# Kernel optimization log

Hardware: AMD Instinct MI355X
Metric: run time of the kernel (lower is better)

Reference implementation:

```python
import jax, jax.numpy as jnp
import numpy as np

N = 172032          # total anchor points (8 images x 21504)
C = 256             # prompt classes
REG_MAX = 16        # DFL bins
M = 64              # GT boxes
IMG = 1024.0
RADIUS = 0.75       # center_sampling_radius
SIGMA = 2.0         # heat sigma
ALPHA, GAMMA = 0.75, 2.0  # varifocal
MARGIN = 8.0
AREA_THR = 0.6
EPS = 1e-6


def setup_inputs() -> dict:
    key = jax.random.key(0)
    ks = jax.random.split(key, 10)
    anchor_points = jax.random.uniform(ks[0], (N, 2)) * IMG
    cls_logits = jax.random.normal(ks[1], (N, C))
    target_scores = jax.random.uniform(ks[2], (N, C))
    pred_dist = jax.random.normal(ks[3], (N, 4, REG_MAX))
    dfl_target = jax.random.uniform(ks[4], (N, 4)) * (REG_MAX - 1)
    # valid xyxy GT boxes inside the image
    xy = jax.random.uniform(ks[5], (M, 2)) * (IMG - 200.0)
    wh = jax.random.uniform(ks[6], (M, 2)) * 180.0 + 20.0
    gt_boxes = jnp.concatenate([xy, xy + wh], axis=-1)
    box_weights = jax.random.uniform(ks[7], (M,))
    pred_boxes = jax.random.uniform(ks[8], (N, 4)) * IMG
    obj_logits = jax.random.normal(ks[9], (N,))
    return {"anchor_points": anchor_points, "cls_logits": cls_logits,
            "target_scores": target_scores, "pred_dist": pred_dist,
            "dfl_target": dfl_target, "gt_boxes": gt_boxes,
            "box_weights": box_weights, "pred_boxes": pred_boxes,
            "obj_logits": obj_logits}


def _inside_and_delta(ap, boxes):
    # ap [N,2], boxes [M,4] -> inside [M,N], delta [M,N,2], half_size [M,1,2]
    inside = ((ap[None, :, 0] >= boxes[:, None, 0]) & (ap[None, :, 0] <= boxes[:, None, 2]) &
              (ap[None, :, 1] >= boxes[:, None, 1]) & (ap[None, :, 1] <= boxes[:, None, 3]))
    center = (boxes[:, :2] + boxes[:, 2:]) * 0.5          # [M,2]
    half = jnp.clip((boxes[:, 2:] - boxes[:, :2]) * 0.5, 1.0)
    delta = (ap[None, :, :] - center[:, None, :]) / half[:, None, :]  # [M,N,2]
    return inside, delta


def build_box_region_weights(ap, boxes, bw, radius):
    inside, delta = _inside_and_delta(ap, boxes)
    center_mask = jnp.max(jnp.abs(delta), axis=-1) <= radius           # [M,N]
    cand = inside & center_mask
    has_cand = jnp.any(cand, axis=1, keepdims=True)
    cand = jnp.where(has_cand, cand, inside)                           # fallback to inside
    return jnp.max(cand.astype(bw.dtype) * bw[:, None], axis=0)        # [N]


def build_center_heat_targets(ap, boxes, sigma):
    sigma = max(float(sigma), 0.001)
    inside, delta = _inside_and_delta(ap, boxes)
    heat = jnp.exp(-0.5 * jnp.sum((delta / sigma) ** 2, axis=-1))      # [M,N]
    heat = heat * inside.astype(heat.dtype)
    return jnp.clip(jnp.max(heat, axis=0), 0.0, 1.0)                   # [N]


def sigmoid_varifocal_loss(logits, targets, alpha, gamma):
    prob = jax.nn.sigmoid(logits)
    weight = alpha * prob ** gamma * (1.0 - targets) + targets
    # stable BCE-with-logits
    bce = jnp.maximum(logits, 0.0) - logits * targets + jnp.log1p(jnp.exp(-jnp.abs(logits)))
    return bce * weight


def dfl_loss(pred_dist, target, reg_max):
    # pred_dist [N,4,R], target [N,4] float in [0, R-1]
    tl = jnp.clip(target.astype(jnp.int32), 0, reg_max - 1)
    tr = jnp.clip(tl + 1, 0, reg_max - 1)
    wl = tr.astype(target.dtype) - target
    wr = 1.0 - wl
    logp = jax.nn.log_softmax(pred_dist, axis=-1)
    ll = -jnp.take_along_axis(logp, tl[..., None], axis=-1)[..., 0]
    lr = -jnp.take_along_axis(logp, tr[..., None], axis=-1)[..., 0]
    return ll * wl + lr * wr                                           # [N,4]


def weighted_mean(loss, weights):
    while weights.ndim < loss.ndim:
        weights = weights[..., None]
    return jnp.sum(loss * weights) / jnp.clip(jnp.sum(weights), EPS)


def oversize_box_penalty(boxes, image_size, area_threshold):
    x1 = jnp.clip(boxes[:, 0], 0.0, image_size)
    y1 = jnp.clip(boxes[:, 1], 0.0, image_size)
    x2 = jnp.clip(boxes[:, 2], 0.0, image_size)
    y2 = jnp.clip(boxes[:, 3], 0.0, image_size)
    w = jnp.clip(x2 - x1, 0.0)
    h = jnp.clip(y2 - y1, 0.0)
    area_ratio = w * h / max(float(image_size * image_size), 1.0)
    edge = ((x1 <= 1.0).astype(boxes.dtype) + (y1 <= 1.0).astype(boxes.dtype) +
            (x2 >= image_size - 1.0).astype(boxes.dtype) + (y2 >= image_size - 1.0).astype(boxes.dtype)) / 4.0
    return jnp.clip(area_ratio - area_threshold, 0.0) * (1.0 + edge)


def reference(anchor_points, cls_logits, target_scores, pred_dist, dfl_target,
              gt_boxes, box_weights, pred_boxes, obj_logits):
    region_w = build_box_region_weights(anchor_points, gt_boxes, box_weights, RADIUS)  # [N]
    heat = build_center_heat_targets(anchor_points, gt_boxes, SIGMA)                   # [N]

    vfl = sigmoid_varifocal_loss(cls_logits, target_scores, ALPHA, GAMMA)              # [N,C]
    cls_loss = weighted_mean(vfl, region_w + heat)

    obj_bce = jnp.maximum(obj_logits, 0.0) - obj_logits * heat + jnp.log1p(jnp.exp(-jnp.abs(obj_logits)))
    obj_loss = jnp.mean(obj_bce)

    dfl = dfl_loss(pred_dist, dfl_target, REG_MAX)                                     # [N,4]
    box_dfl_loss = weighted_mean(dfl, region_w)

    penalty = jnp.mean(oversize_box_penalty(pred_boxes, IMG, AREA_THR))
    margin = jnp.mean(jax.nn.relu(jnp.max(cls_logits, axis=-1) - MARGIN))

    total = cls_loss + obj_loss + box_dfl_loss + 0.1 * penalty + 0.05 * margin
    return total
```

## Files before the change

kernel.cpp:

```cpp
#include <hip/hip_runtime.h>

#define MM 64
#define NQ 7
#define MAIN_BLOCKS 1024

__device__ __forceinline__ float vfl_term(float l, float t, float* lmax) {
    float e = __expf(-l);
    float p = __fdividef(1.0f, 1.0f + e);
    float bce = fmaxf(l, 0.0f) - l * t - __logf(fmaxf(p, 1.0f - p));
    float wgt = 0.75f * p * p * (1.0f - t) + t;
    *lmax = fmaxf(*lmax, l);
    return bce * wgt;
}

__global__ __launch_bounds__(256) void k_hascand(
    const float2* __restrict__ ap, const float4* __restrict__ boxes,
    unsigned long long* __restrict__ mask, int n_pts)
{
    __shared__ float4 sb[MM];
    if (threadIdx.x < MM) sb[threadIdx.x] = boxes[threadIdx.x];
    __syncthreads();
    unsigned long long local = 0ull;
    int stride = gridDim.x * blockDim.x;
    for (int n = blockIdx.x * blockDim.x + threadIdx.x; n < n_pts; n += stride) {
        float2 p = ap[n];
        for (int m = 0; m < MM; ++m) {
            float4 b = sb[m];
            if (p.x >= b.x && p.x <= b.z && p.y >= b.y && p.y <= b.w) {
                float hx = fmaxf((b.z - b.x) * 0.5f, 1.0f);
                float hy = fmaxf((b.w - b.y) * 0.5f, 1.0f);
                float dx = fabsf(p.x - (b.x + b.z) * 0.5f) / hx;
                float dy = fabsf(p.y - (b.y + b.w) * 0.5f) / hy;
                if (fmaxf(dx, dy) <= 0.75f) local |= (1ull << m);
            }
        }
    }
    #pragma unroll
    for (int o = 32; o; o >>= 1) local |= __shfl_xor(local, o);
    if ((threadIdx.x & 63) == 0 && local) atomicOr(mask, local);
}

__global__ __launch_bounds__(256) void k_main(
    const float2* __restrict__ ap,
    const float4* __restrict__ cls4,
    const float4* __restrict__ ts4,
    const float*  __restrict__ pd,
    const float*  __restrict__ dflt,
    const float4* __restrict__ boxes,
    const float*  __restrict__ bw,
    const float4* __restrict__ pboxes,
    const float*  __restrict__ obj,
    const unsigned long long* __restrict__ candmask,
    float* __restrict__ partials,
    int n_pts)
{
    const int tid  = threadIdx.x;
    const int lane = tid & 63;
    const int wid  = tid >> 6;
    const int waveGlobal = blockIdx.x * 4 + wid;
    const int totalWaves = gridDim.x * 4;

    float4 b  = boxes[lane];
    float mybw = bw[lane];
    float inv_hx = __fdividef(1.0f, fmaxf((b.z - b.x) * 0.5f, 1.0f));
    float inv_hy = __fdividef(1.0f, fmaxf((b.w - b.y) * 0.5f, 1.0f));
    float ccx = (b.x + b.z) * 0.5f, ccy = (b.y + b.w) * 0.5f;
    bool has_c = ((candmask[0] >> lane) & 1ull) != 0;

    const int kseg = lane >> 4;
    const int jj   = lane & 15;

    float accS1 = 0.f;
    float accS3 = 0.f;
    float accS2 = 0.f;
    float accS4 = 0.f;
    float accObj = 0.f;
    float accMar = 0.f;

    for (int n = waveGlobal; n < n_pts; n += totalWaves) {
        float2 p = ap[n];
        bool inside = (p.x >= b.x) & (p.x <= b.z) & (p.y >= b.y) & (p.y <= b.w);
        float dx = (p.x - ccx) * inv_hx;
        float dy = (p.y - ccy) * inv_hy;
        bool cand = inside && (fmaxf(fabsf(dx), fabsf(dy)) <= 0.75f);
        bool eff  = has_c ? cand : inside;
        float rw = eff ? mybw : 0.f;
        float ht = inside ? __expf(-0.125f * (dx * dx + dy * dy)) : 0.f;
        #pragma unroll
        for (int o = 32; o; o >>= 1) {
            rw = fmaxf(rw, __shfl_xor(rw, o));
            ht = fmaxf(ht, __shfl_xor(ht, o));
        }
        ht = fminf(ht, 1.0f);
        float w = rw + ht;

        float4 l4 = cls4[(size_t)n * 64 + lane];
        float4 t4 = ts4[(size_t)n * 64 + lane];
        float lmax = -1e30f;
        float vsum = vfl_term(l4.x, t4.x, &lmax) + vfl_term(l4.y, t4.y, &lmax)
                   + vfl_term(l4.z, t4.z, &lmax) + vfl_term(l4.w, t4.w, &lmax);
        accS1 += w * vsum;
        #pragma unroll
        for (int o = 32; o; o >>= 1) lmax = fmaxf(lmax, __shfl_xor(lmax, o));
        accMar += fmaxf(lmax - 8.0f, 0.f);
        accS2 += w;
        accS4 += rw;

        float ol = obj[n];
        accObj += fmaxf(ol, 0.f) - ol * ht + __logf(1.0f + __expf(-fabsf(ol)));

        float x = pd[(size_t)n * 64 + lane];
        float tg = dflt[(size_t)n * 4 + kseg];
        float mx = x;
        #pragma unroll
        for (int o = 8; o; o >>= 1) mx = fmaxf(mx, __shfl_xor(mx, o));
        float e = __expf(x - mx);
        float se = e;
        #pragma unroll
        for (int o = 8; o; o >>= 1) se += __shfl_xor(se, o);
        float logp = (x - mx) - __logf(se);
        int tl = (int)tg; tl = max(0, min(tl, 15));
        int tr = min(tl + 1, 15);
        float wl = (float)tr - tg;
        float contrib = 0.f;
        if (jj == tl) contrib += -logp * wl;
        if (jj == tr) contrib += -logp * (1.0f - wl);
        accS3 += rw * contrib;
    }

    float accPen = 0.f;
    int gsize = gridDim.x * blockDim.x;
    for (int n = blockIdx.x * blockDim.x + tid; n < n_pts; n += gsize) {
        float4 pbx = pboxes[n];
        float x1 = fminf(fmaxf(pbx.x, 0.f), 1024.0f);
        float y1 = fminf(fmaxf(pbx.y, 0.f), 1024.0f);
        float x2 = fminf(fmaxf(pbx.z, 0.f), 1024.0f);
        float y2 = fminf(fmaxf(pbx.w, 0.f), 1024.0f);
        float wq = fmaxf(x2 - x1, 0.f), hq = fmaxf(y2 - y1, 0.f);
        float ar = wq * hq * (1.0f / (1024.0f * 1024.0f));
        float edge = ((x1 <= 1.f ? 1.f : 0.f) + (y1 <= 1.f ? 1.f : 0.f) +
                      (x2 >= 1023.f ? 1.f : 0.f) + (y2 >= 1023.f ? 1.f : 0.f)) * 0.25f;
        accPen += fmaxf(ar - 0.6f, 0.f) * (1.f + edge);
    }

    #pragma unroll
    for (int o = 32; o; o >>= 1) {
        accS1  += __shfl_xor(accS1, o);
        accS3  += __shfl_xor(accS3, o);
        accPen += __shfl_xor(accPen, o);
    }
    __shared__ float sh[4][NQ];
    if (lane == 0) {
        sh[wid][0] = accS1; sh[wid][1] = accS2; sh[wid][2] = accS3;
        sh[wid][3] = accS4; sh[wid][4] = accObj; sh[wid][5] = accMar;
        sh[wid][6] = accPen;
    }
    __syncthreads();
    if (tid < NQ) {
        partials[blockIdx.x * NQ + tid] =
            sh[0][tid] + sh[1][tid] + sh[2][tid] + sh[3][tid];
    }
}

__global__ __launch_bounds__(256) void k_final(
    const float* __restrict__ partials, int nblocks,
    float* __restrict__ out, int n_pts)
{
    double acc[NQ];
    #pragma unroll
    for (int q = 0; q < NQ; ++q) acc[q] = 0.0;
    for (int i = threadIdx.x; i < nblocks; i += 256) {
        #pragma unroll
        for (int q = 0; q < NQ; ++q) acc[q] += (double)partials[i * NQ + q];
    }
    __shared__ double sh[256][NQ + 1];
    #pragma unroll
    for (int q = 0; q < NQ; ++q) sh[threadIdx.x][q] = acc[q];
    __syncthreads();
    for (int s = 128; s; s >>= 1) {
        if (threadIdx.x < s) {
            #pragma unroll
            for (int q = 0; q < NQ; ++q) sh[threadIdx.x][q] += sh[threadIdx.x + s][q];
        }
        __syncthreads();
    }
    if (threadIdx.x == 0) {
        double S1 = sh[0][0], S2 = sh[0][1], S3 = sh[0][2], S4 = sh[0][3];
        double So = sh[0][4], Sm = sh[0][5], Sp = sh[0][6];
        double invN = 1.0 / (double)n_pts;
        double cls_loss = S1 / fmax(S2, 1e-6);
        double dfl_loss = S3 / fmax(S4, 1e-6);
        double total = cls_loss + So * invN + dfl_loss + 0.1 * Sp * invN + 0.05 * Sm * invN;
        out[0] = (float)total;
    }
}

extern "C" void kernel_launch(void* const* d_in, const int* in_sizes, int n_in,
                              void* d_out, int out_size, void* d_ws, size_t ws_size,
                              hipStream_t stream) {
    const float2* ap    = (const float2*)d_in[0];
    const float4* cls4  = (const float4*)d_in[1];
    const float4* ts4   = (const float4*)d_in[2];
    const float*  pd    = (const float*)d_in[3];
    const float*  dflt  = (const float*)d_in[4];
    const float4* boxes = (const float4*)d_in[5];
    const float*  bw    = (const float*)d_in[6];
    const float4* pbx   = (const float4*)d_in[7];
    const float*  obj   = (const float*)d_in[8];
    int n_pts = in_sizes[0] / 2;

    unsigned long long* mask = (unsigned long long*)d_ws;
    float* partials = (float*)((char*)d_ws + 16);

    hipMemsetAsync(d_ws, 0, 16, stream);
    k_hascand<<<256, 256, 0, stream>>>(ap, boxes, mask, n_pts);
    k_main<<<MAIN_BLOCKS, 256, 0, stream>>>(ap, cls4, ts4, pd, dflt, boxes, bw,
                                            pbx, obj, mask, partials, n_pts);
    k_final<<<1, 256, 0, stream>>>(partials, MAIN_BLOCKS, (float*)d_out, n_pts);
}
```

Before: 155.4 us.

## Precompute per-anchor region and heat weights in a prep kernel, unroll main loop

Adds a k_prep kernel that computes each anchor's region weight and heat target by a per-thread loop over the 64 boxes and writes them to a workspace buffer. k_main then loads these weights instead of doing 64-lane box tests and two wave-wide max reductions per anchor. The main loop also handles two anchors per iteration to raise memory-level parallelism, and the grid size is doubled. The cost is an extra kernel launch plus a write and read of a small per-anchor buffer. An unused helper (anchor_body) has a malformed obj term, but it is never called.

```diff
diff --git a/kernel.cpp b/kernel.cpp
--- a/kernel.cpp
+++ b/kernel.cpp
@@ -2,7 +2,7 @@
 
 #define MM 64
 #define NQ 7
-#define MAIN_BLOCKS 1024
+#define MAIN_BLOCKS 2048
 
 __device__ __forceinline__ float vfl_term(float l, float t, float* lmax) {
     float e = __expf(-l);
@@ -40,17 +40,74 @@
     if ((threadIdx.x & 63) == 0 && local) atomicOr(mask, local);
 }
 
+__global__ __launch_bounds__(256) void k_prep(
+    const float2* __restrict__ ap, const float4* __restrict__ boxes,
+    const float* __restrict__ bw, const unsigned long long* __restrict__ candmask,
+    float2* __restrict__ w2, int n_pts)
+{
+    __shared__ float4 sB[MM];
+    __shared__ float4 sA[MM];
+    __shared__ float  sW[MM];
+    if (threadIdx.x < MM) {
+        float4 b = boxes[threadIdx.x];
+        sB[threadIdx.x] = b;
+        float ihx = __fdividef(1.0f, fmaxf((b.z - b.x) * 0.5f, 1.0f));
+        float ihy = __fdividef(1.0f, fmaxf((b.w - b.y) * 0.5f, 1.0f));
+        sA[threadIdx.x] = make_float4((b.x + b.z) * 0.5f, (b.y + b.w) * 0.5f, ihx, ihy);
+        sW[threadIdx.x] = bw[threadIdx.x];
+    }
+    __syncthreads();
+    unsigned long long cm = candmask[0];
+    int stride = gridDim.x * blockDim.x;
+    for (int n = blockIdx.x * blockDim.x + threadIdx.x; n < n_pts; n += stride) {
+        float2 p = ap[n];
+        float rw = 0.f, ht = 0.f;
+        #pragma unroll 8
+        for (int m = 0; m < MM; ++m) {
+            float4 b = sB[m];
+            float4 a = sA[m];
+            bool inside = (p.x >= b.x) & (p.x <= b.z) & (p.y >= b.y) & (p.y <= b.w);
+            float dx = (p.x - a.x) * a.z;
+            float dy = (p.y - a.y) * a.w;
+            bool cand = inside && (fmaxf(fabsf(dx), fabsf(dy)) <= 0.75f);
+            bool eff = ((cm >> m) & 1ull) ? cand : inside;
+            if (eff) rw = fmaxf(rw, sW[m]);
+            float h = __expf(-0.125f * (dx * dx + dy * dy));
+            if (inside) ht = fmaxf(ht, h);
+        }
+        ht = fminf(ht, 1.0f);
+        w2[n] = make_float2(rw + ht, rw);
+    }
+}
+
+__device__ __forceinline__ void anchor_body(
+    float4 l4, float4 t4, float pda, float2 wv, float ol, float tg,
+    int jj, float valid,
+    float* accS1, float* accS2, float* accS3, float* accS4,
+    float* accObj, float* accMar)
+{
+    float w = wv.x, rw = wv.y;
+    float lmax = -1e30f;
+    float vsum = vfl_term(l4.x, t4.x, &lmax) + vfl_term(l4.y, t4.y, &lmax)
+               + vfl_term(l4.z, t4.z, &lmax) + vfl_term(l4.w, t4.w, &lmax);
+    *accS1 += valid * w * vsum;
+    #pragma unroll
+    for (int o = 32; o; o >>= 1) lmax = fmaxf(lmax, __shfl_xor(lmax, o));
+    *accMar += valid * fmaxf(lmax - 8.0f, 0.f);
+    *accS2 += valid * w;
+    *accS4 += valid * rw;
+
+    *accObj += valid * (fmaxf(ol, 0.f) - ol * w , 0.f);
+}
+
 __global__ __launch_bounds__(256) void k_main(
-    const float2* __restrict__ ap,
     const float4* __restrict__ cls4,
     const float4* __restrict__ ts4,
     const float*  __restrict__ pd,
     const float*  __restrict__ dflt,
-    const float4* __restrict__ boxes,
-    const float*  __restrict__ bw,
     const float4* __restrict__ pboxes,
     const float*  __restrict__ obj,
-    const unsigned long long* __restrict__ candmask,
+    const float2* __restrict__ w2,
     float* __restrict__ partials,
     int n_pts)
 {
@@ -58,74 +115,87 @@
     const int lane = tid & 63;
     const int wid  = tid >> 6;
     const int waveGlobal = blockIdx.x * 4 + wid;
-    const int totalWaves = gridDim.x * 4;
-
-    float4 b  = boxes[lane];
-    float mybw = bw[lane];
-    float inv_hx = __fdividef(1.0f, fmaxf((b.z - b.x) * 0.5f, 1.0f));
-    float inv_hy = __fdividef(1.0f, fmaxf((b.w - b.y) * 0.5f, 1.0f));
-    float ccx = (b.x + b.z) * 0.5f, ccy = (b.y + b.w) * 0.5f;
-    bool has_c = ((candmask[0] >> lane) & 1ull) != 0;
+    const int step = gridDim.x * 4;
 
     const int kseg = lane >> 4;
     const int jj   = lane & 15;
 
-    float accS1 = 0.f;
-    float accS3 = 0.f;
-    float accS2 = 0.f;
-    float accS4 = 0.f;
-    float accObj = 0.f;
-    float accMar = 0.f;
-
-    for (int n = waveGlobal; n < n_pts; n += totalWaves) {
-        float2 p = ap[n];
-        bool inside = (p.x >= b.x) & (p.x <= b.z) & (p.y >= b.y) & (p.y <= b.w);
-        float dx = (p.x - ccx) * inv_hx;
-        float dy = (p.y - ccy) * inv_hy;
-        bool cand = inside && (fmaxf(fabsf(dx), fabsf(dy)) <= 0.75f);
-        bool eff  = has_c ? cand : inside;
-        float rw = eff ? mybw : 0.f;
-        float ht = inside ? __expf(-0.125f * (dx * dx + dy * dy)) : 0.f;
-        #pragma unroll
-        for (int o = 32; o; o >>= 1) {
-            rw = fmaxf(rw, __shfl_xor(rw, o));
-            ht = fmaxf(ht, __shfl_xor(ht, o));
-        }
-        ht = fminf(ht, 1.0f);
-        float w = rw + ht;
-
-        float4 l4 = cls4[(size_t)n * 64 + lane];
-        float4 t4 = ts4[(size_t)n * 64 + lane];
-        float lmax = -1e30f;
-        float vsum = vfl_term(l4.x, t4.x, &lmax) + vfl_term(l4.y, t4.y, &lmax)
-                   + vfl_term(l4.z, t4.z, &lmax) + vfl_term(l4.w, t4.w, &lmax);
-        accS1 += w * vsum;
-        #pragma unroll
-        for (int o = 32; o; o >>= 1) lmax = fmaxf(lmax, __shfl_xor(lmax, o));
-        accMar += fmaxf(lmax - 8.0f, 0.f);
-        accS2 += w;
-        accS4 += rw;
-
-        float ol = obj[n];
-        accObj += fmaxf(ol, 0.f) - ol * ht + __logf(1.0f + __expf(-fabsf(ol)));
-
-        float x = pd[(size_t)n * 64 + lane];
-        float tg = dflt[(size_t)n * 4 + kseg];
-        float mx = x;
-        #pragma unroll
-        for (int o = 8; o; o >>= 1) mx = fmaxf(mx, __shfl_xor(mx, o));
-        float e = __expf(x - mx);
-        float se = e;
-        #pragma unroll
-        for (int o = 8; o; o >>= 1) se += __shfl_xor(se, o);
-        float logp = (x - mx) - __logf(se);
-        int tl = (int)tg; tl = max(0, min(tl, 15));
-        int tr = min(tl + 1, 15);
-        float wl = (float)tr - tg;
-        float contrib = 0.f;
-        if (jj == tl) contrib += -logp * wl;
-        if (jj == tr) contrib += -logp * (1.0f - wl);
-        accS3 += rw * contrib;
+    float accS1 = 0.f, accS2 = 0.f, accS3 = 0.f, accS4 = 0.f;
+    float accObj = 0.f, accMar = 0.f;
+
+    for (int n = waveGlobal; n < n_pts; n += 2 * step) {
+        int n1 = n + step;
+        bool have2 = n1 < n_pts;
+        size_t r0 = (size_t)n * 64 + lane;
+        size_t r1 = (size_t)(have2 ? n1 : n) * 64 + lane;
+        int q1 = have2 ? n1 : n;
+
+        float4 l4a = cls4[r0], t4a = ts4[r0];
+        float4 l4b = cls4[r1], t4b = ts4[r1];
+        float  pda = pd[r0],   pdb = pd[r1];
+        float2 wva = w2[n],    wvb = w2[q1];
+        float  ola = obj[n],   olb = obj[q1];
+        float  tga = dflt[(size_t)n * 4 + kseg], tgb = dflt[(size_t)q1 * 4 + kseg];
+        float  v1 = have2 ? 1.0f : 0.0f;
+
+        {
+            float w = wva.x, rw = wva.y, ht = wva.x - wva.y;
+            float lmax = -1e30f;
+            float vsum = vfl_term(l4a.x, t4a.x, &lmax) + vfl_term(l4a.y, t4a.y, &lmax)
+                       + vfl_term(l4a.z, t4a.z, &lmax) + vfl_term(l4a.w, t4a.w, &lmax);
+            accS1 += w * vsum;
+            #pragma unroll
+            for (int o = 32; o; o >>= 1) lmax = fmaxf(lmax, __shfl_xor(lmax, o));
+            accMar += fmaxf(lmax - 8.0f, 0.f);
+            accS2 += w; accS4 += rw;
+            accObj += fmaxf(ola, 0.f) - ola * ht + __logf(1.0f + __expf(-fabsf(ola)));
+
+            float x = pda;
+            float mx = x;
+            #pragma unroll
+            for (int o = 8; o; o >>= 1) mx = fmaxf(mx, __shfl_xor(mx, o));
+            float e = __expf(x - mx);
+            float se = e;
+            #pragma unroll
+            for (int o = 8; o; o >>= 1) se += __shfl_xor(se, o);
+            float logp = (x - mx) - __logf(se);
+            int tl = (int)tga; tl = max(0, min(tl, 15));
+            int tr = min(tl + 1, 15);
+            float wl = (float)tr - tga;
+            float contrib = 0.f;
+            if (jj == tl) contrib += -logp * wl;
+            if (jj == tr) contrib += -logp * (1.0f - wl);
+            accS3 += rw * contrib;
+        }
+        {
+            float w = wvb.x, rw = wvb.y, ht = wvb.x - wvb.y;
+            float lmax = -1e30f;
+            float vsum = vfl_term(l4b.x, t4b.x, &lmax) + vfl_term(l4b.y, t4b.y, &lmax)
+                       + vfl_term(l4b.z, t4b.z, &lmax) + vfl_term(l4b.w, t4b.w, &lmax);
+            accS1 += v1 * w * vsum;
+            #pragma unroll
+            for (int o = 32; o; o >>= 1) lmax = fmaxf(lmax, __shfl_xor(lmax, o));
+            accMar += v1 * fmaxf(lmax - 8.0f, 0.f);
+            accS2 += v1 * w; accS4 += v1 * rw;
+            accObj += v1 * (fmaxf(olb, 0.f) - olb * ht + __logf(1.0f + __expf(-fabsf(olb))));
+
+            float x = pdb;
+            float mx = x;
+            #pragma unroll
+            for (int o = 8; o; o >>= 1) mx = fmaxf(mx, __shfl_xor(mx, o));
+            float e = __expf(x - mx);
+            float se = e;
+            #pragma unroll
+            for (int o = 8; o; o >>= 1) se += __shfl_xor(se, o);
+            float logp = (x - mx) - __logf(se);
+            int tl = (int)tgb; tl = max(0, min(tl, 15));
+            int tr = min(tl + 1, 15);
+            float wl = (float)tr - tgb;
+            float contrib = 0.f;
+            if (jj == tl) contrib += -logp * wl;
+            if (jj == tr) contrib += -logp * (1.0f - wl);
+            accS3 += v1 * rw * contrib;
+        }
     }
 
     float accPen = 0.f;
@@ -210,11 +280,13 @@
     int n_pts = in_sizes[0] / 2;
 
     unsigned long long* mask = (unsigned long long*)d_ws;
-    float* partials = (float*)((char*)d_ws + 16);
+    float* partials = (float*)((char*)d_ws + 64);
+    float2* w2 = (float2*)((char*)d_ws + 65536);
 
     hipMemsetAsync(d_ws, 0, 16, stream);
     k_hascand<<<256, 256, 0, stream>>>(ap, boxes, mask, n_pts);
-    k_main<<<MAIN_BLOCKS, 256, 0, stream>>>(ap, cls4, ts4, pd, dflt, boxes, bw,
-                                            pbx, obj, mask, partials, n_pts);
+    k_prep<<<672, 256, 0, stream>>>(ap, boxes, bw, mask, w2, n_pts);
+    k_main<<<MAIN_BLOCKS, 256, 0, stream>>>(cls4, ts4, pd, dflt, pbx, obj, w2,
+                                            partials, n_pts);
     k_final<<<1, 256, 0, stream>>>(partials, MAIN_BLOCKS, (float*)d_out, n_pts);
 }
```

Result: faster. 150.8 us (-3.0%).

## Split per-point weight computation into prep kernel and batch main loop four points per wave

Applied to the files above, without the earlier changes.

Adds a prep kernel that computes per-point region and heat weights (one thread per point looping over boxes), plus the objectness and penalty terms, and writes the weights to a workspace buffer. The main kernel then only streams the class, target and distribution tensors, handling four points per wave iteration so more loads are in flight. It also drops the max-subtraction in the DFL softmax, rewrites the DFL target as a triangle weight, and skips the margin reduction unless some logit exceeds the margin. The costs are an extra launch and a workspace round trip. Removing the softmax max-subtraction risks overflow for large logits, and the loop stops at multiples of four points, which can drop a tail of points.

```diff
diff --git a/kernel.cpp b/kernel.cpp
--- a/kernel.cpp
+++ b/kernel.cpp
@@ -1,15 +1,18 @@
 #include <hip/hip_runtime.h>
 
 #define MM 64
-#define NQ 7
-#define MAIN_BLOCKS 1024
-
-__device__ __forceinline__ float vfl_term(float l, float t, float* lmax) {
+#define MAIN_BLOCKS 1344
+#define PREP_BLOCKS 672
+#define NQ_MAIN 5
+#define NQ_PREP 2
+
+__device__ __forceinline__ float vfl1(float l, float t, float* vmax) {
     float e = __expf(-l);
     float p = __fdividef(1.0f, 1.0f + e);
-    float bce = fmaxf(l, 0.0f) - l * t - __logf(fmaxf(p, 1.0f - p));
-    float wgt = 0.75f * p * p * (1.0f - t) + t;
-    *lmax = fmaxf(*lmax, l);
+    float q = fmaxf(p, 1.0f - p);
+    float bce = fmaf(-l, t, fmaxf(l, 0.0f)) - __logf(q);
+    float wgt = fmaf(0.75f * p * p, 1.0f - t, t);
+    *vmax = fmaxf(*vmax, l);
     return bce * wgt;
 }
 
@@ -40,97 +43,49 @@
     if ((threadIdx.x & 63) == 0 && local) atomicOr(mask, local);
 }
 
-__global__ __launch_bounds__(256) void k_main(
-    const float2* __restrict__ ap,
-    const float4* __restrict__ cls4,
-    const float4* __restrict__ ts4,
-    const float*  __restrict__ pd,
-    const float*  __restrict__ dflt,
-    const float4* __restrict__ boxes,
-    const float*  __restrict__ bw,
-    const float4* __restrict__ pboxes,
-    const float*  __restrict__ obj,
-    const unsigned long long* __restrict__ candmask,
-    float* __restrict__ partials,
-    int n_pts)
-{
-    const int tid  = threadIdx.x;
-    const int lane = tid & 63;
-    const int wid  = tid >> 6;
-    const int waveGlobal = blockIdx.x * 4 + wid;
-    const int totalWaves = gridDim.x * 4;
-
-    float4 b  = boxes[lane];
-    float mybw = bw[lane];
-    float inv_hx = __fdividef(1.0f, fmaxf((b.z - b.x) * 0.5f, 1.0f));
-    float inv_hy = __fdividef(1.0f, fmaxf((b.w - b.y) * 0.5f, 1.0f));
-    float ccx = (b.x + b.z) * 0.5f, ccy = (b.y + b.w) * 0.5f;
-    bool has_c = ((candmask[0] >> lane) & 1ull) != 0;
-
-    const int kseg = lane >> 4;
-    const int jj   = lane & 15;
-
-    float accS1 = 0.f;
-    float accS3 = 0.f;
-    float accS2 = 0.f;
-    float accS4 = 0.f;
-    float accObj = 0.f;
-    float accMar = 0.f;
-
-    for (int n = waveGlobal; n < n_pts; n += totalWaves) {
+__global__ __launch_bounds__(256) void k_prep(
+    const float2* __restrict__ ap, const float4* __restrict__ boxes,
+    const float* __restrict__ bw, const unsigned long long* __restrict__ candmask,
+    const float4* __restrict__ pboxes, const float* __restrict__ obj,
+    float2* __restrict__ w2, float* __restrict__ prep_partials, int n_pts)
+{
+    __shared__ float4 sB[MM];
+    __shared__ float4 sA[MM];
+    __shared__ float  sW[MM];
+    if (threadIdx.x < MM) {
+        float4 b = boxes[threadIdx.x];
+        sB[threadIdx.x] = b;
+        float ihx = __fdividef(1.0f, fmaxf((b.z - b.x) * 0.5f, 1.0f));
+        float ihy = __fdividef(1.0f, fmaxf((b.w - b.y) * 0.5f, 1.0f));
+        sA[threadIdx.x] = make_float4((b.x + b.z) * 0.5f, (b.y + b.w) * 0.5f, ihx, ihy);
+        sW[threadIdx.x] = bw[threadIdx.x];
+    }
+    __syncthreads();
+    unsigned long long cm = candmask[0];
+    int n = blockIdx.x * blockDim.x + threadIdx.x;
+    float aObj = 0.f, aPen = 0.f;
+    if (n < n_pts) {
         float2 p = ap[n];
-        bool inside = (p.x >= b.x) & (p.x <= b.z) & (p.y >= b.y) & (p.y <= b.w);
-        float dx = (p.x - ccx) * inv_hx;
-        float dy = (p.y - ccy) * inv_hy;
-        bool cand = inside && (fmaxf(fabsf(dx), fabsf(dy)) <= 0.75f);
-        bool eff  = has_c ? cand : inside;
-        float rw = eff ? mybw : 0.f;
-        float ht = inside ? __expf(-0.125f * (dx * dx + dy * dy)) : 0.f;
-        #pragma unroll
-        for (int o = 32; o; o >>= 1) {
-            rw = fmaxf(rw, __shfl_xor(rw, o));
-            ht = fmaxf(ht, __shfl_xor(ht, o));
+        float rw = 0.f, ht = 0.f;
+        #pragma unroll 8
+        for (int m = 0; m < MM; ++m) {
+            float4 b = sB[m];
+            float4 a = sA[m];
+            bool inside = (p.x >= b.x) & (p.x <= b.z) & (p.y >= b.y) & (p.y <= b.w);
+            float dx = (p.x - a.x) * a.z;
+            float dy = (p.y - a.y) * a.w;
+            bool cand = inside && (fmaxf(fabsf(dx), fabsf(dy)) <= 0.75f);
+            bool eff = ((cm >> m) & 1ull) ? cand : inside;
+            if (eff) rw = fmaxf(rw, sW[m]);
+            float h = __expf(-0.125f * (dx * dx + dy * dy));
+            if (inside) ht = fmaxf(ht, h);
         }
         ht = fminf(ht, 1.0f);
-        float w = rw + ht;
-
-        float4 l4 = cls4[(size_t)n * 64 + lane];
-        float4 t4 = ts4[(size_t)n * 64 + lane];
-        float lmax = -1e30f;
-        float vsum = vfl_term(l4.x, t4.x, &lmax) + vfl_term(l4.y, t4.y, &lmax)
-                   + vfl_term(l4.z, t4.z, &lmax) + vfl_term(l4.w, t4.w, &lmax);
-        accS1 += w * vsum;
-        #pragma unroll
-        for (int o = 32; o; o >>= 1) lmax = fmaxf(lmax, __shfl_xor(lmax, o));
-        accMar += fmaxf(lmax - 8.0f, 0.f);
-        accS2 += w;
-        accS4 += rw;
+        w2[n] = make_float2(rw + ht, rw);
 
         float ol = obj[n];
-        accObj += fmaxf(ol, 0.f) - ol * ht + __logf(1.0f + __expf(-fabsf(ol)));
-
-        float x = pd[(size_t)n * 64 + lane];
-        float tg = dflt[(size_t)n * 4 + kseg];
-        float mx = x;
-        #pragma unroll
-        for (int o = 8; o; o >>= 1) mx = fmaxf(mx, __shfl_xor(mx, o));
-        float e = __expf(x - mx);
-        float se = e;
-        #pragma unroll
-        for (int o = 8; o; o >>= 1) se += __shfl_xor(se, o);
-        float logp = (x - mx) - __logf(se);
-        int tl = (int)tg; tl = max(0, min(tl, 15));
-        int tr = min(tl + 1, 15);
-        float wl = (float)tr - tg;
-        float contrib = 0.f;
-        if (jj == tl) contrib += -logp * wl;
-        if (jj == tr) contrib += -logp * (1.0f - wl);
-        accS3 += rw * contrib;
-    }
-
-    float accPen = 0.f;
-    int gsize = gridDim.x * blockDim.x;
-    for (int n = blockIdx.x * blockDim.x + tid; n < n_pts; n += gsize) {
+        aObj = fmaxf(ol, 0.f) - ol * ht + __logf(1.0f + __expf(-fabsf(ol)));
+
         float4 pbx = pboxes[n];
         float x1 = fminf(fmaxf(pbx.x, 0.f), 1024.0f);
         float y1 = fminf(fmaxf(pbx.y, 0.f), 1024.0f);
@@ -140,58 +95,133 @@
         float ar = wq * hq * (1.0f / (1024.0f * 1024.0f));
         float edge = ((x1 <= 1.f ? 1.f : 0.f) + (y1 <= 1.f ? 1.f : 0.f) +
                       (x2 >= 1023.f ? 1.f : 0.f) + (y2 >= 1023.f ? 1.f : 0.f)) * 0.25f;
-        accPen += fmaxf(ar - 0.6f, 0.f) * (1.f + edge);
-    }
-
+        aPen = fmaxf(ar - 0.6f, 0.f) * (1.f + edge);
+    }
     #pragma unroll
     for (int o = 32; o; o >>= 1) {
-        accS1  += __shfl_xor(accS1, o);
-        accS3  += __shfl_xor(accS3, o);
-        accPen += __shfl_xor(accPen, o);
-    }
-    __shared__ float sh[4][NQ];
+        aObj += __shfl_xor(aObj, o);
+        aPen += __shfl_xor(aPen, o);
+    }
+    __shared__ float sh[4][2];
+    int lane = threadIdx.x & 63, wid = threadIdx.x >> 6;
+    if (lane == 0) { sh[wid][0] = aObj; sh[wid][1] = aPen; }
+    __syncthreads();
+    if (threadIdx.x < NQ_PREP) {
+        prep_partials[blockIdx.x * NQ_PREP + threadIdx.x] =
+            sh[0][threadIdx.x] + sh[1][threadIdx.x] + sh[2][threadIdx.x] + sh[3][threadIdx.x];
+    }
+}
+
+__global__ __launch_bounds__(256) void k_main(
+    const float4* __restrict__ cls4,
+    const float4* __restrict__ ts4,
+    const float*  __restrict__ pd,
+    const float*  __restrict__ dflt,
+    const float2* __restrict__ w2,
+    float* __restrict__ partials,
+    int n_pts)
+{
+    const int tid  = threadIdx.x;
+    const int lane = tid & 63;
+    const int wid  = tid >> 6;
+    const int wave = blockIdx.x * 4 + wid;
+    const int CHUNK = MAIN_BLOCKS * 4 * 4;
+    const int ksel = lane >> 4;
+    const float jjf = (float)(lane & 15);
+
+    float accS1 = 0.f, accS2 = 0.f, accS3 = 0.f, accS4 = 0.f, accMar = 0.f;
+
+    for (int n0 = wave * 4; n0 + 3 < n_pts; n0 += CHUNK) {
+        float4 l4[4], t4[4];
+        float  xp[4], tg[4];
+        float2 wv[4];
+        #pragma unroll
+        for (int u = 0; u < 4; ++u) {
+            int n = n0 + u;
+            int o = n * 64 + lane;
+            l4[u] = cls4[o];
+            t4[u] = ts4[o];
+            xp[u] = pd[o];
+            wv[u] = w2[n];
+            tg[u] = dflt[n * 4 + ksel];
+        }
+        #pragma unroll
+        for (int u = 0; u < 4; ++u) {
+            float w = wv[u].x, rw = wv[u].y;
+            float vmax = -1e30f;
+            float vsum = vfl1(l4[u].x, t4[u].x, &vmax) + vfl1(l4[u].y, t4[u].y, &vmax)
+                       + vfl1(l4[u].z, t4[u].z, &vmax) + vfl1(l4[u].w, t4[u].w, &vmax);
+            accS1 = fmaf(w, vsum, accS1);
+            accS2 += w;
+            accS4 += rw;
+            if (__any(vmax > 8.0f)) {
+                float t = vmax;
+                #pragma unroll
+                for (int o = 32; o; o >>= 1) t = fmaxf(t, __shfl_xor(t, o));
+                accMar += t - 8.0f;
+            }
+            float e = __expf(xp[u]);
+            float se = e;
+            #pragma unroll
+            for (int o = 8; o; o >>= 1) se += __shfl_xor(se, o);
+            float lse = __logf(se);
+            float d  = tg[u] - jjf;
+            float tw = fmaxf(1.0f - fabsf(d), 0.0f);
+            float term = fmaf(-tw, xp[u], lse * 0.0625f);
+            accS3 = fmaf(rw, term, accS3);
+        }
+    }
+
+    #pragma unroll
+    for (int o = 32; o; o >>= 1) {
+        accS1 += __shfl_xor(accS1, o);
+        accS3 += __shfl_xor(accS3, o);
+    }
+    __shared__ float sh[4][NQ_MAIN];
     if (lane == 0) {
         sh[wid][0] = accS1; sh[wid][1] = accS2; sh[wid][2] = accS3;
-        sh[wid][3] = accS4; sh[wid][4] = accObj; sh[wid][5] = accMar;
-        sh[wid][6] = accPen;
-    }
-    __syncthreads();
-    if (tid < NQ) {
-        partials[blockIdx.x * NQ + tid] =
+        sh[wid][3] = accS4; sh[wid][4] = accMar;
+    }
+    __syncthreads();
+    if (tid < NQ_MAIN) {
+        partials[blockIdx.x * NQ_MAIN + tid] =
             sh[0][tid] + sh[1][tid] + sh[2][tid] + sh[3][tid];
     }
 }
 
 __global__ __launch_bounds__(256) void k_final(
-    const float* __restrict__ partials, int nblocks,
+    const float* __restrict__ mainp, const float* __restrict__ prepp,
     float* __restrict__ out, int n_pts)
 {
-    double acc[NQ];
-    #pragma unroll
-    for (int q = 0; q < NQ; ++q) acc[q] = 0.0;
-    for (int i = threadIdx.x; i < nblocks; i += 256) {
-        #pragma unroll
-        for (int q = 0; q < NQ; ++q) acc[q] += (double)partials[i * NQ + q];
-    }
-    __shared__ double sh[256][NQ + 1];
-    #pragma unroll
-    for (int q = 0; q < NQ; ++q) sh[threadIdx.x][q] = acc[q];
+    double acc[7];
+    #pragma unroll
+    for (int q = 0; q < 7; ++q) acc[q] = 0.0;
+    for (int i = threadIdx.x; i < MAIN_BLOCKS; i += 256) {
+        #pragma unroll
+        for (int q = 0; q < NQ_MAIN; ++q) acc[q] += (double)mainp[i * NQ_MAIN + q];
+    }
+    for (int i = threadIdx.x; i < PREP_BLOCKS; i += 256) {
+        #pragma unroll
+        for (int q = 0; q < NQ_PREP; ++q) acc[5 + q] += (double)prepp[i * NQ_PREP + q];
+    }
+    __shared__ double sh[256][8];
+    #pragma unroll
+    for (int q = 0; q < 7; ++q) sh[threadIdx.x][q] = acc[q];
     __syncthreads();
     for (int s = 128; s; s >>= 1) {
         if (threadIdx.x < s) {
             #pragma unroll
-            for (int q = 0; q < NQ; ++q) sh[threadIdx.x][q] += sh[threadIdx.x + s][q];
+            for (int q = 0; q < 7; ++q) sh[threadIdx.x][q] += sh[threadIdx.x + s][q];
         }
         __syncthreads();
     }
     if (threadIdx.x == 0) {
         double S1 = sh[0][0], S2 = sh[0][1], S3 = sh[0][2], S4 = sh[0][3];
-        double So = sh[0][4], Sm = sh[0][5], Sp = sh[0][6];
+        double Sm = sh[0][4], So = sh[0][5], Sp = sh[0][6];
         double invN = 1.0 / (double)n_pts;
         double cls_loss = S1 / fmax(S2, 1e-6);
         double dfl_loss = S3 / fmax(S4, 1e-6);
-        double total = cls_loss + So * invN + dfl_loss + 0.1 * Sp * invN + 0.05 * Sm * invN;
-        out[0] = (float)total;
+        out[0] = (float)(cls_loss + So * invN + dfl_loss + 0.1 * Sp * invN + 0.05 * Sm * invN);
     }
 }
 
@@ -210,11 +240,15 @@
     int n_pts = in_sizes[0] / 2;
 
     unsigned long long* mask = (unsigned long long*)d_ws;
-    float* partials = (float*)((char*)d_ws + 16);
+    float* main_partials = (float*)((char*)d_ws + 1024);
+    float* prep_partials = (float*)((char*)d_ws + 32768);
+    float2* w2 = (float2*)((char*)d_ws + 65536);
 
     hipMemsetAsync(d_ws, 0, 16, stream);
     k_hascand<<<256, 256, 0, stream>>>(ap, boxes, mask, n_pts);
-    k_main<<<MAIN_BLOCKS, 256, 0, stream>>>(ap, cls4, ts4, pd, dflt, boxes, bw,
-                                            pbx, obj, mask, partials, n_pts);
-    k_final<<<1, 256, 0, stream>>>(partials, MAIN_BLOCKS, (float*)d_out, n_pts);
-}
+    k_prep<<<PREP_BLOCKS, 256, 0, stream>>>(ap, boxes, bw, mask, pbx, obj, w2,
+                                            prep_partials, n_pts);
+    k_main<<<MAIN_BLOCKS, 256, 0, stream>>>(cls4, ts4, pd, dflt, w2,
+                                            main_partials, n_pts);
+    k_final<<<1, 256, 0, stream>>>(main_partials, prep_partials, (float*)d_out, n_pts);
+}
```

Result: faster. 144.7 us (-6.9%).
